# Kernel optimization log

Hardware: AMD Instinct MI355X
Metric: run time of the kernel (lower is better)

The kernel has to match this reference:

```python
import jax, jax.numpy as jnp
import numpy as np

N_NODES = 100000
N_GRAPHS = 512
NEG_SLOPE = 0.2
EPS = 1e-16


def gat_conv(x, W, a_src, a_dst, bias, src, dst, heads, out_ch, concat):
    # x: [N, Fin]; W: [Fin, heads*out_ch]; a_src/a_dst: [heads, out_ch]
    N = x.shape[0]
    h = (x @ W).reshape(N, heads, out_ch)                      # [N,H,C]
    alpha_src = jnp.einsum('nhc,hc->nh', h, a_src)             # [N,H]
    alpha_dst = jnp.einsum('nhc,hc->nh', h, a_dst)             # [N,H]
    e = alpha_src[src] + alpha_dst[dst]                        # [E,H]
    e = jnp.where(e > 0, e, NEG_SLOPE * e)                     # leaky relu
    # segment softmax over incoming edges per destination node
    m = jax.ops.segment_max(e, dst, num_segments=N)            # [N,H]
    m = jnp.where(jnp.isfinite(m), m, 0.0)
    ee = jnp.exp(e - m[dst])
    denom = jax.ops.segment_sum(ee, dst, num_segments=N)       # [N,H]
    alpha = ee / (denom[dst] + EPS)                            # [E,H]
    msg = h[src] * alpha[:, :, None]                           # [E,H,C]
    out = jax.ops.segment_sum(msg, dst, num_segments=N)        # [N,H,C]
    if concat:
        out = out.reshape(N, heads * out_ch)
    else:
        out = out.mean(axis=1)
    return out + bias


def setup_inputs() -> dict:
    key = jax.random.key(0)
    ks = jax.random.split(key, 12)
    x = jax.random.normal(ks[0], (N_NODES, 128), dtype=jnp.float32)
    edge_index = jax.random.randint(ks[1], (2, 1600000), 0, N_NODES, dtype=jnp.int64)
    batch = jnp.sort(jax.random.randint(ks[2], (N_NODES,), 0, N_GRAPHS, dtype=jnp.int64))
    s = 0.1
    W1 = jax.random.normal(ks[3], (128, 64), dtype=jnp.float32) * s
    a_src1 = jax.random.normal(ks[4], (8, 8), dtype=jnp.float32) * s
    a_dst1 = jax.random.normal(ks[5], (8, 8), dtype=jnp.float32) * s
    b1 = jnp.zeros((64,), dtype=jnp.float32)
    W2 = jax.random.normal(ks[6], (64, 10), dtype=jnp.float32) * s
    a_src2 = jax.random.normal(ks[7], (1, 10), dtype=jnp.float32) * s
    a_dst2 = jax.random.normal(ks[8], (1, 10), dtype=jnp.float32) * s
    b2 = jnp.zeros((10,), dtype=jnp.float32)
    return {"x": x, "edge_index": edge_index, "batch": batch,
            "W1": W1, "a_src1": a_src1, "a_dst1": a_dst1, "b1": b1,
            "W2": W2, "a_src2": a_src2, "a_dst2": a_dst2, "b2": b2}


def reference(x, edge_index, batch, W1, a_src1, a_dst1, b1, W2, a_src2, a_dst2, b2):
    N = x.shape[0]
    # PyG GATConv default add_self_loops=True
    loops = jnp.arange(N, dtype=edge_index.dtype)
    src = jnp.concatenate([edge_index[0], loops])
    dst = jnp.concatenate([edge_index[1], loops])
    # eval mode: dropout layers are identity
    h = gat_conv(x, W1, a_src1, a_dst1, b1, src, dst, heads=8, out_ch=8, concat=True)
    h = jax.nn.elu(h)
    h = gat_conv(h, W2, a_src2, a_dst2, b2, src, dst, heads=1, out_ch=10, concat=False)
    # global mean pool over graphs
    sums = jax.ops.segment_sum(h, batch, num_segments=N_GRAPHS)        # [G,10]
    cnts = jax.ops.segment_sum(jnp.ones((N, 1), h.dtype), batch, num_segments=N_GRAPHS)
    pooled = sums / jnp.maximum(cnts, 1.0)
    return jax.nn.log_softmax(pooled, axis=1)
```

## Files before the change

### kernel.cpp

```cpp
#include <hip/hip_runtime.h>
#include <math.h>

#define L2E 1.44269504088896f
#define LRELU(v) fmaxf((v), 0.2f * (v))

__device__ __forceinline__ float fexp2(float v) { return __builtin_amdgcn_exp2f(v); }
__device__ __forceinline__ float felu(float r) {
    return r > 0.f ? r : fexp2(r * L2E) - 1.f;
}

__device__ __forceinline__ unsigned short f2bf(float f) {
    unsigned u = __float_as_uint(f);
    u += 0x7FFFu + ((u >> 16) & 1u);
    return (unsigned short)(u >> 16);
}
__device__ __forceinline__ float bf2f(unsigned short b) {
    return __uint_as_float((unsigned)b << 16);
}

typedef __attribute__((ext_vector_type(8))) short bf16x8;
typedef __attribute__((ext_vector_type(4))) float f32x4;

#define UPD8(mm, dd, Aa, Ab, ev, U)                                       \
    {                                                                     \
        float mn_ = fmaxf(mm, ev);                                        \
        float sc_ = fexp2(mm - mn_);                                      \
        float w_  = fexp2(ev - mn_);                                      \
        dd = dd * sc_ + w_;                                               \
        Aa.x = Aa.x * sc_ + w_ * __uint_as_float((U).x << 16);            \
        Aa.y = Aa.y * sc_ + w_ * __uint_as_float((U).x & 0xffff0000u);    \
        Aa.z = Aa.z * sc_ + w_ * __uint_as_float((U).y << 16);            \
        Aa.w = Aa.w * sc_ + w_ * __uint_as_float((U).y & 0xffff0000u);    \
        Ab.x = Ab.x * sc_ + w_ * __uint_as_float((U).z << 16);            \
        Ab.y = Ab.y * sc_ + w_ * __uint_as_float((U).z & 0xffff0000u);    \
        Ab.z = Ab.z * sc_ + w_ * __uint_as_float((U).w << 16);            \
        Ab.w = Ab.w * sc_ + w_ * __uint_as_float((U).w & 0xffff0000u);    \
        mm = mn_;                                                         \
    }
#define UPD1(mm, dd, aa, ev, hv)           \
    {                                      \
        float mn_ = fmaxf(mm, ev);         \
        float sc_ = fexp2(mm - mn_);       \
        float w_  = fexp2(ev - mn_);       \
        dd = dd * sc_ + w_;                \
        aa = aa * sc_ + w_ * (hv);         \
        mm = mn_;                          \
    }

#define CH 4096

__global__ __launch_bounds__(256) void k_gemm1_mfma(
        const float* __restrict__ x, const float* __restrict__ W,
        const float* __restrict__ a_src, const float* __restrict__ a_dst,
        unsigned short* __restrict__ h1b, unsigned short* __restrict__ asrcb,
        float* __restrict__ adst1, int N, int ntiles) {
    int tid = threadIdx.x;
    int w = tid >> 6, l = tid & 63;
    int c0 = w * 16;
    int lr = l & 15;
    int lg = l >> 4;

    bf16x8 bfr[4];
#pragma unroll
    for (int kk = 0; kk < 4; ++kk)
#pragma unroll
        for (int j = 0; j < 8; ++j)
            bfr[kk][j] = (short)f2bf(W[(size_t)(kk * 32 + lg * 8 + j) * 64 + c0 + lr]);

    float asv = a_src[c0 + lr];
    float adv = a_dst[c0 + lr];

    for (int t = blockIdx.x; t < ntiles; t += gridDim.x) {
        int n0 = t * 16;
        int n = n0 + lr;
        const float4* xr = (const float4*)(x + (size_t)(n < N ? n : 0) * 128);
        f32x4 acc = {0.f, 0.f, 0.f, 0.f};
#pragma unroll
        for (int kk = 0; kk < 4; ++kk) {
            float4 u0 = xr[kk * 8 + lg * 2];
            float4 u1 = xr[kk * 8 + lg * 2 + 1];
            bf16x8 afr;
            afr[0] = (short)f2bf(u0.x); afr[1] = (short)f2bf(u0.y);
            afr[2] = (short)f2bf(u0.z); afr[3] = (short)f2bf(u0.w);
            afr[4] = (short)f2bf(u1.x); afr[5] = (short)f2bf(u1.y);
            afr[6] = (short)f2bf(u1.z); afr[7] = (short)f2bf(u1.w);
            acc = __builtin_amdgcn_mfma_f32_16x16x32_bf16(afr, bfr[kk], acc, 0, 0, 0);
        }
#pragma unroll
        for (int r = 0; r < 4; ++r) {
            int nn = n0 + lg * 4 + r;
            if (nn < N) h1b[(size_t)nn * 64 + c0 + lr] = f2bf(acc[r]);
        }
        float ps[4], pd[4];
#pragma unroll
        for (int r = 0; r < 4; ++r) { ps[r] = acc[r] * asv; pd[r] = acc[r] * adv; }
#pragma unroll
        for (int mask = 1; mask <= 4; mask <<= 1)
#pragma unroll
            for (int r = 0; r < 4; ++r) {
                ps[r] += __shfl_xor(ps[r], mask);
                pd[r] += __shfl_xor(pd[r], mask);
            }
        if ((lr & 7) == 0) {
            int h = (c0 + lr) >> 3;
#pragma unroll
            for (int r = 0; r < 4; ++r) {
                int nn = n0 + lg * 4 + r;
                if (nn < N) {
                    asrcb[nn * 8 + h] = f2bf(ps[r] * L2E);
                    adst1[nn * 8 + h] = pd[r] * L2E;
                }
            }
        }
    }
}


__global__ __launch_bounds__(256) void k_bhist(const int* __restrict__ dstE,
                                               const int* __restrict__ batch,
                                               int E, int NB, int G, int* __restrict__ bh) {
    __shared__ int lh[512];
    int tid = threadIdx.x, b = blockIdx.x;
    lh[tid] = 0; lh[tid + 256] = 0;
    __syncthreads();
#pragma unroll
    for (int i = 0; i < CH / 1024; ++i) {
        int eb = b * CH + (i * 256 + tid) * 4;
        if (eb + 3 < E) {
            int4 dv = *(const int4*)(dstE + eb);
            int g0 = batch[dv.x], g1 = batch[dv.y], g2 = batch[dv.z], g3 = batch[dv.w];
            atomicAdd(&lh[g0], 1); atomicAdd(&lh[g1], 1);
            atomicAdd(&lh[g2], 1); atomicAdd(&lh[g3], 1);
        } else {
#pragma unroll
            for (int k = 0; k < 4; ++k)
                if (eb + k < E) atomicAdd(&lh[batch[dstE[eb + k]]], 1);
        }
    }
    __syncthreads();
    if (tid < G)       bh[(size_t)tid * NB + b] = lh[tid];
    if (tid + 256 < G) bh[(size_t)(tid + 256) * NB + b] = lh[tid + 256];
}

__global__ __launch_bounds__(512) void k_mscan(const int* __restrict__ bh, int NB,
                                               int* __restrict__ pstart, int* __restrict__ total) {
    __shared__ int buf[512];
    int bin = blockIdx.x, t = threadIdx.x;
    int v = (t < NB) ? bh[(size_t)bin * NB + t] : 0;
    buf[t] = v;
    __syncthreads();
    for (int off = 1; off < 512; off <<= 1) {
        int u = (t >= off) ? buf[t - off] : 0;
        __syncthreads();
        buf[t] += u;
        __syncthreads();
    }
    if (t < NB) pstart[(size_t)bin * NB + t] = buf[t] - v;
    if (t == 511) total[bin] = buf[511];
}

__global__ __launch_bounds__(1024) void k_scan_top(const int* __restrict__ total, int nb,
                                                   int* __restrict__ boff,
                                                   const int* __restrict__ batch, int N,
                                                   int* __restrict__ nstart) {
    __shared__ int buf[1024];
    int t = threadIdx.x;
    int v = (t < nb) ? total[t] : 0;
    buf[t] = v;
    __syncthreads();
    for (int off = 1; off < 1024; off <<= 1) {
        int u = (t >= off) ? buf[t - off] : 0;
        __syncthreads();
        buf[t] += u;
        __syncthreads();
    }
    if (t < nb) {
        boff[t] = buf[t] - v;
        int lo = 0, hi = N;
        while (lo < hi) { int mid = (lo + hi) >> 1; if (batch[mid] < t) lo = mid + 1; else hi = mid; }
        nstart[t] = lo;
    }
}

__global__ __launch_bounds__(256) void k_bscatter(const int* __restrict__ srcE,
                                                  const int* __restrict__ dstE,
                                                  const int* __restrict__ batch,
                                                  const int* __restrict__ boff,
                                                  const int* __restrict__ pstart,
                                                  const int* __restrict__ nstart,
                                                  int E, int NB, int G, int* __restrict__ pairs) {
    __shared__ int lstart[512];
    __shared__ int lc[512];
    __shared__ int lns[512];
    int tid = threadIdx.x, b = blockIdx.x;
#pragma unroll
    for (int j = tid; j < 512; j += 256) {
        lstart[j] = (j < G) ? boff[j] + pstart[(size_t)j * NB + b] : 0;
        lns[j] = (j < G) ? nstart[j] : 0;
        lc[j] = 0;
    }
    __syncthreads();
#pragma unroll
    for (int i = 0; i < CH / 1024; ++i) {
        int eb = b * CH + (i * 256 + tid) * 4;
        if (eb + 3 < E) {
            int4 sv = *(const int4*)(srcE + eb);
            int4 dv = *(const int4*)(dstE + eb);
            int g0 = batch[dv.x], g1 = batch[dv.y], g2 = batch[dv.z], g3 = batch[dv.w];
            int p0 = atomicAdd(&lc[g0], 1);
            int p1 = atomicAdd(&lc[g1], 1);
            int p2 = atomicAdd(&lc[g2], 1);
            int p3 = atomicAdd(&lc[g3], 1);
            pairs[lstart[g0] + p0] = sv.x | ((dv.x - lns[g0]) << 17);
            pairs[lstart[g1] + p1] = sv.y | ((dv.y - lns[g1]) << 17);
            pairs[lstart[g2] + p2] = sv.z | ((dv.z - lns[g2]) << 17);
            pairs[lstart[g3] + p3] = sv.w | ((dv.w - lns[g3]) << 17);
        } else {
#pragma unroll
            for (int k = 0; k < 4; ++k)
                if (eb + k < E) {
                    int s = srcE[eb + k], d = dstE[eb + k];
                    int bin = batch[d];
                    int old = atomicAdd(&lc[bin], 1);
                    pairs[lstart[bin] + old] = s | ((d - lns[bin]) << 17);
                }
        }
    }
}

__global__ __launch_bounds__(512) void k_csr_local(const int* __restrict__ pairs,
                                                   const int* __restrict__ boff,
                                                   const int* __restrict__ batch,
                                                   int E, int N, int G,
                                                   int* __restrict__ cnt, int* __restrict__ excl,
                                                   int* __restrict__ srcs) {
    __shared__ int lcnt[512];
    __shared__ int buf[512];
    __shared__ int lcur[512];
    int g = blockIdx.x, t = threadIdx.x;
    int lo = 0, hi = N;
    while (lo < hi) { int mid = (lo + hi) >> 1; if (batch[mid] < g) lo = mid + 1; else hi = mid; }
    int ns = lo;
    hi = N;
    while (lo < hi) { int mid = (lo + hi) >> 1; if (batch[mid] < g + 1) lo = mid + 1; else hi = mid; }
    int ne = lo;
    int lnodes = ne - ns;
    int es = boff[g];
    int ee = (g + 1 < G) ? boff[g + 1] : E;

    lcnt[t] = 0;
    __syncthreads();
    for (int e = es + t; e < ee; e += 512) atomicAdd(&lcnt[pairs[e] >> 17], 1);
    __syncthreads();
    int v = lcnt[t];
    buf[t] = v;
    __syncthreads();
    for (int off = 1; off < 512; off <<= 1) {
        int u = (t >= off) ? buf[t - off] : 0;
        __syncthreads();
        buf[t] += u;
        __syncthreads();
    }
    int lex = buf[t] - v;
    lcur[t] = lex;
    if (t < lnodes) {
        cnt[ns + t] = v;
        excl[ns + t] = es + lex;
    }
    __syncthreads();
    for (int e = es + t; e < ee; e += 512) {
        int pv = pairs[e];
        int pos = atomicAdd(&lcur[pv >> 17], 1);
        srcs[es + pos] = pv & 0x1FFFF;
    }
}

__global__ void k_gather1(const int* __restrict__ srcs, const int* __restrict__ excl,
                          const int* __restrict__ cnt,
                          const unsigned short* __restrict__ asrcb, const float* __restrict__ adst1,
                          const unsigned short* __restrict__ h1b,
                          const float* __restrict__ b1, const float* __restrict__ W2,
                          const float* __restrict__ a_src2, const float* __restrict__ a_dst2,
                          unsigned short* __restrict__ h2b, unsigned short* __restrict__ asrc2b,
                          float* __restrict__ adst2, int N) {
    int tid = blockIdx.x * 256 + threadIdx.x;
    int wave = tid >> 6;
    int lane = threadIdx.x & 63;
    int q = lane >> 3;
    int l = lane & 7;
    int wid = wave * 8 + q;
    if (wid >= N) return;
    int c0 = l * 8;

    int beg = excl[wid];
    int cw  = cnt[wid];
    const int* sp = srcs + beg;
    float adh = adst1[wid * 8 + l];

    uint4 us = *(const uint4*)&h1b[(size_t)wid * 64 + c0];
    float4 A0a, A0b;
    A0a.x = __uint_as_float(us.x << 16); A0a.y = __uint_as_float(us.x & 0xffff0000u);
    A0a.z = __uint_as_float(us.y << 16); A0a.w = __uint_as_float(us.y & 0xffff0000u);
    A0b.x = __uint_as_float(us.z << 16); A0b.y = __uint_as_float(us.z & 0xffff0000u);
    A0b.z = __uint_as_float(us.w << 16); A0b.w = __uint_as_float(us.w & 0xffff0000u);
    float m0 = LRELU(bf2f(asrcb[wid * 8 + l]) + adh), d0 = 1.f;
    float4 Z = {0.f, 0.f, 0.f, 0.f};
    float4 A1a = Z, A1b = Z, A2a = Z, A2b = Z, A3a = Z, A3b = Z;
    float m1 = -INFINITY, d1 = 0.f;
    float m2 = -INFINITY, d2 = 0.f;
    float m3 = -INFINITY, d3 = 0.f;

    int i = 0;
    for (; i + 4 <= cw; i += 4) {
        int s0 = sp[i], s1 = sp[i + 1], s2 = sp[i + 2], s3 = sp[i + 3];
        float e0 = LRELU(bf2f(asrcb[s0 * 8 + l]) + adh);
        float e1 = LRELU(bf2f(asrcb[s1 * 8 + l]) + adh);
        float e2 = LRELU(bf2f(asrcb[s2 * 8 + l]) + adh);
        float e3 = LRELU(bf2f(asrcb[s3 * 8 + l]) + adh);
        uint4 u0 = *(const uint4*)&h1b[(size_t)s0 * 64 + c0];
        uint4 u1 = *(const uint4*)&h1b[(size_t)s1 * 64 + c0];
        uint4 u2 = *(const uint4*)&h1b[(size_t)s2 * 64 + c0];
        uint4 u3 = *(const uint4*)&h1b[(size_t)s3 * 64 + c0];
        UPD8(m0, d0, A0a, A0b, e0, u0);
        UPD8(m1, d1, A1a, A1b, e1, u1);
        UPD8(m2, d2, A2a, A2b, e2, u2);
        UPD8(m3, d3, A3a, A3b, e3, u3);
    }
    for (; i < cw; ++i) {
        int s = sp[i];
        float ev = LRELU(bf2f(asrcb[s * 8 + l]) + adh);
        uint4 uv = *(const uint4*)&h1b[(size_t)s * 64 + c0];
        UPD8(m0, d0, A0a, A0b, ev, uv);
    }
    float mM = fmaxf(fmaxf(m0, m1), fmaxf(m2, m3));
    float w0 = fexp2(m0 - mM), w1 = fexp2(m1 - mM);
    float w2 = fexp2(m2 - mM), w3 = fexp2(m3 - mM);
    float den = d0 * w0 + d1 * w1 + d2 * w2 + d3 * w3;
    float inv = 1.f / (den + 1e-16f);
    float rv[8];
    rv[0] = (A0a.x * w0 + A1a.x * w1 + A2a.x * w2 + A3a.x * w3) * inv;
    rv[1] = (A0a.y * w0 + A1a.y * w1 + A2a.y * w2 + A3a.y * w3) * inv;
    rv[2] = (A0a.z * w0 + A1a.z * w1 + A2a.z * w2 + A3a.z * w3) * inv;
    rv[3] = (A0a.w * w0 + A1a.w * w1 + A2a.w * w2 + A3a.w * w3) * inv;
    rv[4] = (A0b.x * w0 + A1b.x * w1 + A2b.x * w2 + A3b.x * w3) * inv;
    rv[5] = (A0b.y * w0 + A1b.y * w1 + A2b.y * w2 + A3b.y * w3) * inv;
    rv[6] = (A0b.z * w0 + A1b.z * w1 + A2b.z * w2 + A3b.z * w3) * inv;
    rv[7] = (A0b.w * w0 + A1b.w * w1 + A2b.w * w2 + A3b.w * w3) * inv;

    float accj[10];
#pragma unroll
    for (int j = 0; j < 10; ++j) accj[j] = 0.f;
#pragma unroll
    for (int t = 0; t < 8; ++t) {
        float r = felu(rv[t] + b1[c0 + t]);
        const float* wr = W2 + (c0 + t) * 10;
#pragma unroll
        for (int j = 0; j < 10; ++j) accj[j] = fmaf(r, wr[j], accj[j]);
    }
#pragma unroll
    for (int mask = 1; mask <= 4; mask <<= 1)
#pragma unroll
        for (int j = 0; j < 10; ++j) accj[j] += __shfl_xor(accj[j], mask);

    if (l == 0) {
        float s = 0.f, d = 0.f;
        unsigned pw[5];
#pragma unroll
        for (int j = 0; j < 10; j += 2) {
            s = fmaf(accj[j], a_src2[j], s);     d = fmaf(accj[j], a_dst2[j], d);
            s = fmaf(accj[j+1], a_src2[j+1], s); d = fmaf(accj[j+1], a_dst2[j+1], d);
            pw[j >> 1] = (unsigned)f2bf(accj[j]) | ((unsigned)f2bf(accj[j+1]) << 16);
        }
        unsigned* hw = (unsigned*)&h2b[(size_t)wid * 10];
#pragma unroll
        for (int j = 0; j < 5; ++j) hw[j] = pw[j];
        asrc2b[wid] = f2bf(s * L2E);
        adst2[wid] = d * L2E;
    }
}

__global__ void k_gather2(const int* __restrict__ srcs, const int* __restrict__ excl,
                          const int* __restrict__ cnt,
                          const unsigned short* __restrict__ asrc2b, const float* __restrict__ adst2,
                          const unsigned short* __restrict__ h2b, float* __restrict__ agg2, int N) {
    int tid = blockIdx.x * 256 + threadIdx.x;
    int wave = tid >> 6;
    int lane = threadIdx.x & 63;
    int q = lane >> 4;
    int l = lane & 15;
    int wid = wave * 4 + q;
    if (wid >= N) return;

    int beg = excl[wid];
    int cw  = cnt[wid];
    const int* sp = srcs + beg;
    float adn = adst2[wid];
    bool ld = l < 10;

    float m0 = LRELU(bf2f(asrc2b[wid]) + adn), d0 = 1.f;
    float a0 = ld ? bf2f(h2b[(size_t)wid * 10 + l]) : 0.f;
    float m1 = -INFINITY, d1 = 0.f, a1 = 0.f;
    float m2 = -INFINITY, d2 = 0.f, a2 = 0.f;
    float m3 = -INFINITY, d3 = 0.f, a3 = 0.f;

    int i = 0;
    for (; i + 4 <= cw; i += 4) {
        int s0 = sp[i], s1 = sp[i + 1], s2 = sp[i + 2], s3 = sp[i + 3];
        float e0 = LRELU(bf2f(asrc2b[s0]) + adn);
        float e1 = LRELU(bf2f(asrc2b[s1]) + adn);
        float e2 = LRELU(bf2f(asrc2b[s2]) + adn);
        float e3 = LRELU(bf2f(asrc2b[s3]) + adn);
        float g0 = ld ? bf2f(h2b[(size_t)s0 * 10 + l]) : 0.f;
        float g1 = ld ? bf2f(h2b[(size_t)s1 * 10 + l]) : 0.f;
        float g2 = ld ? bf2f(h2b[(size_t)s2 * 10 + l]) : 0.f;
        float g3 = ld ? bf2f(h2b[(size_t)s3 * 10 + l]) : 0.f;
        UPD1(m0, d0, a0, e0, g0);
        UPD1(m1, d1, a1, e1, g1);
        UPD1(m2, d2, a2, e2, g2);
        UPD1(m3, d3, a3, e3, g3);
    }
    for (; i < cw; ++i) {
        int s = sp[i];
        float ev = LRELU(bf2f(asrc2b[s]) + adn);
        float gv = ld ? bf2f(h2b[(size_t)s * 10 + l]) : 0.f;
        UPD1(m0, d0, a0, ev, gv);
    }
    float mM = fmaxf(fmaxf(m0, m1), fmaxf(m2, m3));
    float w0 = fexp2(m0 - mM), w1 = fexp2(m1 - mM);
    float w2 = fexp2(m2 - mM), w3 = fexp2(m3 - mM);
    float den = d0 * w0 + d1 * w1 + d2 * w2 + d3 * w3;
    float acc = a0 * w0 + a1 * w1 + a2 * w2 + a3 * w3;
    if (ld) agg2[(size_t)wid * 10 + l] = acc / (den + 1e-16f);
}

__global__ void k_pool_final(const float* __restrict__ agg2, const float* __restrict__ b2,
                             const int* __restrict__ batch, float* __restrict__ out,
                             int N, int G) {
    int g = blockIdx.x;
    int lo = 0, hi = N;
    while (lo < hi) { int mid = (lo + hi) >> 1; if (batch[mid] < g) lo = mid + 1; else hi = mid; }
    int s = lo;
    lo = s; hi = N;
    while (lo < hi) { int mid = (lo + hi) >> 1; if (batch[mid] < g + 1) lo = mid + 1; else hi = mid; }
    int e = lo;
    int tid = threadIdx.x;
    float acc[10];
#pragma unroll
    for (int j = 0; j < 10; ++j) acc[j] = 0.f;
    for (int n = s + tid; n < e; n += 256) {
        const float* r = agg2 + (size_t)n * 10;
#pragma unroll
        for (int j = 0; j < 10; ++j) acc[j] += r[j];
    }
    __shared__ float red[256 * 10];
#pragma unroll
    for (int j = 0; j < 10; ++j) red[tid * 10 + j] = acc[j];
    __syncthreads();
    for (int st = 128; st > 0; st >>= 1) {
        if (tid < st)
#pragma unroll
            for (int j = 0; j < 10; ++j) red[tid * 10 + j] += red[(tid + st) * 10 + j];
        __syncthreads();
    }
    if (tid == 0) {
        int c = e - s;
        float v[10], m = -1e30f;
#pragma unroll
        for (int j = 0; j < 10; ++j) {
            v[j] = (c > 0) ? red[j] / (float)c + b2[j] : 0.f;
            m = fmaxf(m, v[j]);
        }
        float ssum = 0.f;
#pragma unroll
        for (int j = 0; j < 10; ++j) ssum += expf(v[j] - m);
        float ls = logf(ssum);
#pragma unroll
        for (int j = 0; j < 10; ++j) out[(size_t)g * 10 + j] = v[j] - m - ls;
    }
}

extern "C" void kernel_launch(void* const* d_in, const int* in_sizes, int n_in,
                              void* d_out, int out_size, void* d_ws, size_t ws_size,
                              hipStream_t stream) {
    const float* x     = (const float*)d_in[0];
    const int*   ei    = (const int*)d_in[1];
    const int*   batch = (const int*)d_in[2];
    const float* W1    = (const float*)d_in[3];
    const float* as1w  = (const float*)d_in[4];
    const float* ad1w  = (const float*)d_in[5];
    const float* b1    = (const float*)d_in[6];
    const float* W2    = (const float*)d_in[7];
    const float* as2w  = (const float*)d_in[8];
    const float* ad2w  = (const float*)d_in[9];
    const float* b2    = (const float*)d_in[10];

    const int N  = in_sizes[0] / 128;
    const int E  = in_sizes[1] / 2;
    const int G  = out_size / 10;
    const int* srcE = ei;
    const int* dstE = ei + E;

    auto cdiv = [](long long a, long long b) { return (int)((a + b - 1) / b); };
    const int NB = cdiv(E, CH);

    size_t Nz = (size_t)N;
    unsigned short* h1b = (unsigned short*)d_ws;
    float* agg2  = (float*)d_ws;
    unsigned short* asrc1b = h1b + Nz * 64;
    float* adst1 = (float*)(asrc1b + Nz * 8);
    unsigned short* h2b = (unsigned short*)(adst1 + Nz * 8);
    unsigned short* asrc2b = h2b + Nz * 10;
    float* adst2 = (float*)(asrc2b + Nz + (Nz & 1));
    int* pairsA  = (int*)(adst2 + Nz);
    int* cntA    = pairsA + (size_t)E;
    int* exclA   = cntA + Nz;
    int* srcsA   = exclA + Nz;
    int* bhA     = srcsA + E;
    int* pstartA = bhA + (size_t)512 * NB;
    int* totalA  = pstartA + (size_t)512 * NB;
    int* boffA   = totalA + 512;
    int* nstartA = boffA + 512;

    const int B = 256;

    int ntiles = cdiv(N, 16);
    int gB = ntiles < 2048 ? ntiles : 2048;
    k_gemm1_mfma<<<gB, B, 0, stream>>>(x, W1, as1w, ad1w, h1b, asrc1b, adst1, N, ntiles);

    k_bhist<<<NB, B, 0, stream>>>(dstE, batch, E, NB, G, bhA);
    k_mscan<<<512, 512, 0, stream>>>(bhA, NB, pstartA, totalA);
    k_scan_top<<<1, 1024, 0, stream>>>(totalA, G, boffA, batch, N, nstartA);
    k_bscatter<<<NB, B, 0, stream>>>(srcE, dstE, batch, boffA, pstartA, nstartA, E, NB, G, pairsA);
    k_csr_local<<<G, 512, 0, stream>>>(pairsA, boffA, batch, E, N, G, cntA, exclA, srcsA);

    k_gather1<<<cdiv(N, 32), B, 0, stream>>>(srcsA, exclA, cntA, asrc1b, adst1, h1b,
                                             b1, W2, as2w, ad2w, h2b, asrc2b, adst2, N);

    k_gather2<<<cdiv(N, 16), B, 0, stream>>>(srcsA, exclA, cntA, asrc2b, adst2, h2b, agg2, N);

    k_pool_final<<<G, B, 0, stream>>>(agg2, b2, batch, (float*)d_out, N, G);
}
```

Baseline: 187.8 us.

## Fuse global mean pooling into layer-2 gather via per-block atomics

Layer-2 gather kernel now reduces its per-node outputs within each block by graph id and atomically adds partial sums into a pooled buffer, instead of writing agg2 to memory and running a separate per-graph pooling kernel with binary searches. The pooled buffer is zeroed in the existing top-scan kernel, and a small final kernel applies bias, mean and log-softmax using precomputed node starts. This removes an N×10 write and re-read plus one reduction pass. In exchange it adds a block-wide sync and float atomics, which make the summation order nondeterministic.

```diff
diff --git a/kernel.cpp b/kernel.cpp
--- a/kernel.cpp
+++ b/kernel.cpp
@@ -162,7 +162,8 @@
 __global__ __launch_bounds__(1024) void k_scan_top(const int* __restrict__ total, int nb,
                                                    int* __restrict__ boff,
                                                    const int* __restrict__ batch, int N,
-                                                   int* __restrict__ nstart) {
+                                                   int* __restrict__ nstart,
+                                                   float* __restrict__ pooled, int G) {
     __shared__ int buf[1024];
     int t = threadIdx.x;
     int v = (t < nb) ? total[t] : 0;
@@ -180,6 +181,7 @@
         while (lo < hi) { int mid = (lo + hi) >> 1; if (batch[mid] < t) lo = mid + 1; else hi = mid; }
         nstart[t] = lo;
     }
+    for (int i = t; i < G * 10; i += 1024) pooled[i] = 0.f;
 }
 
 __global__ __launch_bounds__(256) void k_bscatter(const int* __restrict__ srcE,
@@ -379,104 +381,106 @@
     }
 }
 
-__global__ void k_gather2(const int* __restrict__ srcs, const int* __restrict__ excl,
-                          const int* __restrict__ cnt,
-                          const unsigned short* __restrict__ asrc2b, const float* __restrict__ adst2,
-                          const unsigned short* __restrict__ h2b, float* __restrict__ agg2, int N) {
+__global__ void k_gather2p(const int* __restrict__ srcs, const int* __restrict__ excl,
+                           const int* __restrict__ cnt,
+                           const unsigned short* __restrict__ asrc2b, const float* __restrict__ adst2,
+                           const unsigned short* __restrict__ h2b,
+                           const int* __restrict__ batch, float* __restrict__ pooled, int N) {
+    __shared__ float lval[16][10];
+    __shared__ int lgr[16];
     int tid = blockIdx.x * 256 + threadIdx.x;
     int wave = tid >> 6;
     int lane = threadIdx.x & 63;
     int q = lane >> 4;
     int l = lane & 15;
     int wid = wave * 4 + q;
-    if (wid >= N) return;
-
-    int beg = excl[wid];
-    int cw  = cnt[wid];
-    const int* sp = srcs + beg;
-    float adn = adst2[wid];
-    bool ld = l < 10;
-
-    float m0 = LRELU(bf2f(asrc2b[wid]) + adn), d0 = 1.f;
-    float a0 = ld ? bf2f(h2b[(size_t)wid * 10 + l]) : 0.f;
-    float m1 = -INFINITY, d1 = 0.f, a1 = 0.f;
-    float m2 = -INFINITY, d2 = 0.f, a2 = 0.f;
-    float m3 = -INFINITY, d3 = 0.f, a3 = 0.f;
-
-    int i = 0;
-    for (; i + 4 <= cw; i += 4) {
-        int s0 = sp[i], s1 = sp[i + 1], s2 = sp[i + 2], s3 = sp[i + 3];
-        float e0 = LRELU(bf2f(asrc2b[s0]) + adn);
-        float e1 = LRELU(bf2f(asrc2b[s1]) + adn);
-        float e2 = LRELU(bf2f(asrc2b[s2]) + adn);
-        float e3 = LRELU(bf2f(asrc2b[s3]) + adn);
-        float g0 = ld ? bf2f(h2b[(size_t)s0 * 10 + l]) : 0.f;
-        float g1 = ld ? bf2f(h2b[(size_t)s1 * 10 + l]) : 0.f;
-        float g2 = ld ? bf2f(h2b[(size_t)s2 * 10 + l]) : 0.f;
-        float g3 = ld ? bf2f(h2b[(size_t)s3 * 10 + l]) : 0.f;
-        UPD1(m0, d0, a0, e0, g0);
-        UPD1(m1, d1, a1, e1, g1);
-        UPD1(m2, d2, a2, e2, g2);
-        UPD1(m3, d3, a3, e3, g3);
-    }
-    for (; i < cw; ++i) {
-        int s = sp[i];
-        float ev = LRELU(bf2f(asrc2b[s]) + adn);
-        float gv = ld ? bf2f(h2b[(size_t)s * 10 + l]) : 0.f;
-        UPD1(m0, d0, a0, ev, gv);
-    }
-    float mM = fmaxf(fmaxf(m0, m1), fmaxf(m2, m3));
-    float w0 = fexp2(m0 - mM), w1 = fexp2(m1 - mM);
-    float w2 = fexp2(m2 - mM), w3 = fexp2(m3 - mM);
-    float den = d0 * w0 + d1 * w1 + d2 * w2 + d3 * w3;
-    float acc = a0 * w0 + a1 * w1 + a2 * w2 + a3 * w3;
-    if (ld) agg2[(size_t)wid * 10 + l] = acc / (den + 1e-16f);
-}
-
-__global__ void k_pool_final(const float* __restrict__ agg2, const float* __restrict__ b2,
-                             const int* __restrict__ batch, float* __restrict__ out,
-                             int N, int G) {
-    int g = blockIdx.x;
-    int lo = 0, hi = N;
-    while (lo < hi) { int mid = (lo + hi) >> 1; if (batch[mid] < g) lo = mid + 1; else hi = mid; }
-    int s = lo;
-    lo = s; hi = N;
-    while (lo < hi) { int mid = (lo + hi) >> 1; if (batch[mid] < g + 1) lo = mid + 1; else hi = mid; }
-    int e = lo;
-    int tid = threadIdx.x;
-    float acc[10];
-#pragma unroll
-    for (int j = 0; j < 10; ++j) acc[j] = 0.f;
-    for (int n = s + tid; n < e; n += 256) {
-        const float* r = agg2 + (size_t)n * 10;
-#pragma unroll
-        for (int j = 0; j < 10; ++j) acc[j] += r[j];
-    }
-    __shared__ float red[256 * 10];
-#pragma unroll
-    for (int j = 0; j < 10; ++j) red[tid * 10 + j] = acc[j];
-    __syncthreads();
-    for (int st = 128; st > 0; st >>= 1) {
-        if (tid < st)
-#pragma unroll
-            for (int j = 0; j < 10; ++j) red[tid * 10 + j] += red[(tid + st) * 10 + j];
-        __syncthreads();
-    }
-    if (tid == 0) {
-        int c = e - s;
-        float v[10], m = -1e30f;
-#pragma unroll
-        for (int j = 0; j < 10; ++j) {
-            v[j] = (c > 0) ? red[j] / (float)c + b2[j] : 0.f;
-            m = fmaxf(m, v[j]);
-        }
-        float ssum = 0.f;
-#pragma unroll
-        for (int j = 0; j < 10; ++j) ssum += expf(v[j] - m);
-        float ls = logf(ssum);
-#pragma unroll
-        for (int j = 0; j < 10; ++j) out[(size_t)g * 10 + j] = v[j] - m - ls;
-    }
+    bool valid = wid < N;
+    if (threadIdx.x < 16) lgr[threadIdx.x] = -1;
+    __syncthreads();
+
+    if (valid) {
+        int beg = excl[wid];
+        int cw  = cnt[wid];
+        const int* sp = srcs + beg;
+        float adn = adst2[wid];
+        bool ld = l < 10;
+
+        float m0 = LRELU(bf2f(asrc2b[wid]) + adn), d0 = 1.f;
+        float a0 = ld ? bf2f(h2b[(size_t)wid * 10 + l]) : 0.f;
+        float m1 = -INFINITY, d1 = 0.f, a1 = 0.f;
+        float m2 = -INFINITY, d2 = 0.f, a2 = 0.f;
+        float m3 = -INFINITY, d3 = 0.f, a3 = 0.f;
+
+        int i = 0;
+        for (; i + 4 <= cw; i += 4) {
+            int s0 = sp[i], s1 = sp[i + 1], s2 = sp[i + 2], s3 = sp[i + 3];
+            float e0 = LRELU(bf2f(asrc2b[s0]) + adn);
+            float e1 = LRELU(bf2f(asrc2b[s1]) + adn);
+            float e2 = LRELU(bf2f(asrc2b[s2]) + adn);
+            float e3 = LRELU(bf2f(asrc2b[s3]) + adn);
+            float g0 = ld ? bf2f(h2b[(size_t)s0 * 10 + l]) : 0.f;
+            float g1 = ld ? bf2f(h2b[(size_t)s1 * 10 + l]) : 0.f;
+            float g2 = ld ? bf2f(h2b[(size_t)s2 * 10 + l]) : 0.f;
+            float g3 = ld ? bf2f(h2b[(size_t)s3 * 10 + l]) : 0.f;
+            UPD1(m0, d0, a0, e0, g0);
+            UPD1(m1, d1, a1, e1, g1);
+            UPD1(m2, d2, a2, e2, g2);
+            UPD1(m3, d3, a3, e3, g3);
+        }
+        for (; i < cw; ++i) {
+            int s = sp[i];
+            float ev = LRELU(bf2f(asrc2b[s]) + adn);
+            float gv = ld ? bf2f(h2b[(size_t)s * 10 + l]) : 0.f;
+            UPD1(m0, d0, a0, ev, gv);
+        }
+        float mM = fmaxf(fmaxf(m0, m1), fmaxf(m2, m3));
+        float w0 = fexp2(m0 - mM), w1 = fexp2(m1 - mM);
+        float w2 = fexp2(m2 - mM), w3 = fexp2(m3 - mM);
+        float den = d0 * w0 + d1 * w1 + d2 * w2 + d3 * w3;
+        float acc = a0 * w0 + a1 * w1 + a2 * w2 + a3 * w3;
+        int slot = wid & 15;
+        if (ld) lval[slot][l] = acc / (den + 1e-16f);
+        if (l == 0) lgr[slot] = batch[wid];
+    }
+    __syncthreads();
+    if (threadIdx.x < 10) {
+        int c = threadIdx.x;
+        float run = 0.f;
+        int curg = -1;
+        for (int s = 0; s < 16; ++s) {
+            int g = lgr[s];
+            if (g < 0) continue;
+            if (g != curg) {
+                if (curg >= 0) atomicAdd(&pooled[curg * 10 + c], run);
+                curg = g; run = 0.f;
+            }
+            run += lval[s][c];
+        }
+        if (curg >= 0) atomicAdd(&pooled[curg * 10 + c], run);
+    }
+}
+
+__global__ __launch_bounds__(512) void k_final(const float* __restrict__ pooled,
+                                               const float* __restrict__ b2,
+                                               const int* __restrict__ nstart,
+                                               float* __restrict__ out, int N, int G) {
+    int t = threadIdx.x + blockIdx.x * 512;
+    if (t >= G) return;
+    int c = ((t + 1 < G) ? nstart[t + 1] : N) - nstart[t];
+    float cf = (float)c;
+    float invc = 1.f / fmaxf(cf, 1.f);
+    float v[10], m = -1e30f;
+#pragma unroll
+    for (int j = 0; j < 10; ++j) {
+        v[j] = (pooled[(size_t)t * 10 + j] + cf * b2[j]) * invc;
+        m = fmaxf(m, v[j]);
+    }
+    float ssum = 0.f;
+#pragma unroll
+    for (int j = 0; j < 10; ++j) ssum += expf(v[j] - m);
+    float ls = logf(ssum);
+#pragma unroll
+    for (int j = 0; j < 10; ++j) out[(size_t)t * 10 + j] = v[j] - m - ls;
 }
 
 extern "C" void kernel_launch(void* const* d_in, const int* in_sizes, int n_in,
@@ -505,7 +509,6 @@
 
     size_t Nz = (size_t)N;
     unsigned short* h1b = (unsigned short*)d_ws;
-    float* agg2  = (float*)d_ws;
     unsigned short* asrc1b = h1b + Nz * 64;
     float* adst1 = (float*)(asrc1b + Nz * 8);
     unsigned short* h2b = (unsigned short*)(adst1 + Nz * 8);
@@ -520,6 +523,7 @@
     int* totalA  = pstartA + (size_t)512 * NB;
     int* boffA   = totalA + 512;
     int* nstartA = boffA + 512;
+    float* pooledA = (float*)(nstartA + 512);
 
     const int B = 256;
 
@@ -529,14 +533,15 @@
 
     k_bhist<<<NB, B, 0, stream>>>(dstE, batch, E, NB, G, bhA);
     k_mscan<<<512, 512, 0, stream>>>(bhA, NB, pstartA, totalA);
-    k_scan_top<<<1, 1024, 0, stream>>>(totalA, G, boffA, batch, N, nstartA);
+    k_scan_top<<<1, 1024, 0, stream>>>(totalA, G, boffA, batch, N, nstartA, pooledA, G);
     k_bscatter<<<NB, B, 0, stream>>>(srcE, dstE, batch, boffA, pstartA, nstartA, E, NB, G, pairsA);
     k_csr_local<<<G, 512, 0, stream>>>(pairsA, boffA, batch, E, N, G, cntA, exclA, srcsA);
 
     k_gather1<<<cdiv(N, 32), B, 0, stream>>>(srcsA, exclA, cntA, asrc1b, adst1, h1b,
                                              b1, W2, as2w, ad2w, h2b, asrc2b, adst2, N);
 
-    k_gather2<<<cdiv(N, 16), B, 0, stream>>>(srcsA, exclA, cntA, asrc2b, adst2, h2b, agg2, N);
-
-    k_pool_final<<<G, B, 0, stream>>>(agg2, b2, batch, (float*)d_out, N, G);
-}
+    k_gather2p<<<cdiv(N, 16), B, 0, stream>>>(srcsA, exclA, cntA, asrc2b, adst2, h2b,
+                                              batch, pooledA, N);
+
+    k_final<<<cdiv(G, 512), 512, 0, stream>>>(pooledA, b2, nstartA, (float*)d_out, N, G);
+}
```

Measured after the change: 184.8 us. No clear change (-1.6%).
